# Performance work log

Measured on AMD Instinct MI355X. Metric: run time of the kernel, lower is better.

Reference implementation:

```python
import jax, jax.numpy as jnp
import numpy as np

N = 500_000      # total nodes in batched graph
B = 2_048        # number of graphs (segments)
D = 256          # input_dim == hidden_dim == output_dim


def setup_inputs() -> dict:
    key = jax.random.key(0)
    k = jax.random.split(key, 8)
    feat = jax.random.normal(k[0], (N, D), dtype=jnp.float32)
    cnt = jax.random.uniform(k[1], (N,), dtype=jnp.float32)
    segment_ids = jnp.sort(jax.random.randint(k[2], (N,), 0, B, dtype=jnp.int32))
    last_nodes = jax.random.randint(k[3], (B,), 0, N, dtype=jnp.int32)
    # learned parameters (torch nn.Linear: y = x @ W.T + b)
    s = 1.0 / np.sqrt(D)
    W_u = jax.random.uniform(k[4], (D, D), dtype=jnp.float32, minval=-s, maxval=s)
    W_v = jax.random.uniform(k[5], (D, D), dtype=jnp.float32, minval=-s, maxval=s)
    b_v = jax.random.uniform(k[6], (D,), dtype=jnp.float32, minval=-s, maxval=s)
    w_e = jax.random.uniform(k[7], (D,), dtype=jnp.float32, minval=-s, maxval=s)
    return {"feat": feat, "cnt": cnt, "segment_ids": segment_ids,
            "last_nodes": last_nodes, "W_u": W_u, "W_v": W_v,
            "b_v": b_v, "w_e": w_e}


def reference(feat, cnt, segment_ids, last_nodes, W_u, W_v, b_v, w_e):
    # fc_u: per-node projection  [N, D]
    feat_u = feat @ W_u.T
    # fc_v on last node of each graph, then broadcast back to nodes
    feat_v = feat[last_nodes] @ W_v.T + b_v          # [B, D]
    feat_vb = feat_v[segment_ids]                    # [N, D] broadcast_nodes
    # fc_e(sigmoid(u + v)) -> scalar gate per node
    e = jax.nn.sigmoid(feat_u + feat_vb) @ w_e       # [N]
    alpha = e * cnt                                  # [N]
    # segment-sum readout over graphs
    rst = jax.ops.segment_sum(feat * alpha[:, None], segment_ids,
                              num_segments=B)        # [B, D]
    return rst
```

## Files before the change

kernel.cpp:

```cpp
#include <hip/hip_runtime.h>
#include <hip/hip_bf16.h>

typedef __attribute__((ext_vector_type(8))) short short8;
typedef __attribute__((ext_vector_type(4))) float f32x4;

#define D 256
#define MT 64
#define NW 8
#define GRID_MAIN 512
#define G 16

__device__ __forceinline__ unsigned pack2(float a, float b) {
    __hip_bfloat162 h = __float22bfloat162_rn(make_float2(a, b));
    return *(unsigned*)&h;
}
__device__ __forceinline__ float fast_sigmoid(float x) {
    return __builtin_amdgcn_rcpf(1.f + __expf(-x));
}

__global__ __launch_bounds__(256) void k_prep(
    const float* __restrict__ W, unsigned short* __restrict__ Wb,
    float* __restrict__ rst, int nW, int nOut) {
    int b = blockIdx.x;
    if (b < 256) {
        int i = b * 256 + threadIdx.x;
        if (i < nW) Wb[i] = (unsigned short)(pack2(W[i], 0.f) & 0xffffu);
    } else {
        int i = (b - 256) * 256 + threadIdx.x;
        if (i < nOut) rst[i] = 0.f;
    }
}

__global__ __launch_bounds__(256) void k_featv(
    const float* __restrict__ feat, const int* __restrict__ last_nodes,
    const float* __restrict__ Wv, const float* __restrict__ bv,
    float* __restrict__ featv, int Bseg) {
    __shared__ float fln[G][D];
    const int t  = threadIdx.x;
    const int b0 = blockIdx.x * G;
    for (int g = 0; g < G; ++g) {
        int b = b0 + g;
        int ln = (b < Bseg) ? last_nodes[b] : 0;
        fln[g][t] = feat[(long)ln * D + t];
    }
    __syncthreads();
    float acc[G];
    float bvj = bv[t];
    #pragma unroll
    for (int g = 0; g < G; ++g) acc[g] = bvj;
    const float* wr = Wv + (long)t * D;
    for (int k = 0; k < D; k += 4) {
        float4 w4 = *(const float4*)(wr + k);
        #pragma unroll
        for (int g = 0; g < G; ++g) {
            acc[g] += w4.x * fln[g][k]     + w4.y * fln[g][k + 1]
                    + w4.z * fln[g][k + 2] + w4.w * fln[g][k + 3];
        }
    }
    for (int g = 0; g < G; ++g)
        if (b0 + g < Bseg) featv[(long)(b0 + g) * D + t] = acc[g];
}

__global__ __launch_bounds__(512, 2) void k_main(
    const float* __restrict__ feat, const float* __restrict__ cnt,
    const int* __restrict__ seg, const unsigned short* __restrict__ Wub,
    const float* __restrict__ featv, const float* __restrict__ we,
    float* __restrict__ rst, int N) {

    __shared__ unsigned short Abuf[2][MT][D];
    __shared__ float e_s[NW][MT];
    __shared__ int   seg_s[2][MT];
    __shared__ float cnt_s[2][MT];
    __shared__ float alpha_s[MT];

    const int t  = threadIdx.x;
    const int w  = t >> 6;
    const int l  = t & 63;
    const int rl = l & 15;
    const int h  = l >> 4;

    const int T   = (N + MT - 1) / MT;
    const int nb  = gridDim.x;
    const int per = T / nb, rem = T % nb;
    const int bid = blockIdx.x;
    const int c0  = bid * per + (bid < rem ? bid : rem);
    const int c1  = c0 + per + (bid < rem ? 1 : 0);
    if (c0 >= c1) return;

    short8 a_reg[2][8];
    {
        const unsigned short* ab = Wub + (long)(32 * w + rl) * D + h * 8;
        #pragma unroll
        for (int mt = 0; mt < 2; ++mt)
            #pragma unroll
            for (int s = 0; s < 8; ++s)
                a_reg[mt][s] = *(const short8*)(ab + (long)mt * 16 * D + s * 32);
    }
    f32x4 wev[2];
    wev[0] = *(const f32x4*)(we + 32 * w + h * 4);
    wev[1] = *(const f32x4*)(we + 32 * w + 16 + h * 4);

    {
        const long m0 = (long)c0 * MT;
        float4 sv[8];
        #pragma unroll
        for (int k = 0; k < 8; ++k) {
            long n = m0 + w * 8 + k; if (n > (long)N - 1) n = (long)N - 1;
            sv[k] = *(const float4*)(feat + n * D + 4 * l);
        }
        int sr = 0; float cr = 0.f;
        if (t < MT) {
            long n = m0 + t;
            if (n < N) { sr = seg[n]; cr = cnt[n]; }
            else       { sr = seg[N - 1]; cr = 0.f; }
        }
        #pragma unroll
        for (int k = 0; k < 8; ++k) {
            int R = w * 8 + k;
            uint2 v = make_uint2(pack2(sv[k].x, sv[k].y), pack2(sv[k].z, sv[k].w));
            *(uint2*)&Abuf[0][R][(((l >> 1) ^ k) << 3) + (l & 1) * 4] = v;
        }
        if (t < MT) { seg_s[0][t] = sr; cnt_s[0][t] = cr; }
        __syncthreads();
    }

    int cur = 0;
    for (int tt = c0; tt < c1; ++tt, cur ^= 1) {
        const int n0  = tt * MT;
        const int nv  = min(MT, N - n0);
        const bool more = (tt + 1 < c1);
        const int* seg_t = seg_s[cur];

        int sgv[4];
        #pragma unroll
        for (int nt = 0; nt < 4; ++nt) sgv[nt] = seg_t[nt * 16 + rl];

        f32x4 fvr[2][4];
        #pragma unroll
        for (int nt = 0; nt < 4; ++nt) {
            const float* fb = featv + (long)sgv[nt] * D + 32 * w + h * 4;
            fvr[0][nt] = *(const f32x4*)(fb);
            fvr[1][nt] = *(const f32x4*)(fb + 16);
        }
        asm volatile("" ::: "memory");

        float4 sv[8];
        int sr = 0; float cr = 0.f;
        if (more) {
            const long m1 = (long)(tt + 1) * MT;
            #pragma unroll
            for (int k = 0; k < 8; ++k) {
                long n = m1 + w * 8 + k; if (n > (long)N - 1) n = (long)N - 1;
                sv[k] = *(const float4*)(feat + n * D + 4 * l);
            }
            if (t < MT) {
                long n = m1 + t;
                if (n < N) { sr = seg[n]; cr = cnt[n]; }
                else       { sr = seg[N - 1]; cr = 0.f; }
            }
        }
        asm volatile("" ::: "memory");

        f32x4 acc[2][4];
        #pragma unroll
        for (int mt = 0; mt < 2; ++mt)
            #pragma unroll
            for (int nt = 0; nt < 4; ++nt) acc[mt][nt] = (f32x4)0.f;

        const unsigned short* Ab = &Abuf[cur][0][0];
        __builtin_amdgcn_s_setprio(1);
        #pragma unroll
        for (int s = 0; s < 8; ++s) {
            short8 bfr[4];
            #pragma unroll
            for (int nt = 0; nt < 4; ++nt) {
                int R = nt * 16 + rl;
                int gr = (s * 4 + h) ^ (rl & 7);
                bfr[nt] = *(const short8*)(Ab + R * D + gr * 8);
            }
            #pragma unroll
            for (int mt = 0; mt < 2; ++mt)
                #pragma unroll
                for (int nt = 0; nt < 4; ++nt)
                    acc[mt][nt] = __builtin_amdgcn_mfma_f32_16x16x32_bf16(a_reg[mt][s], bfr[nt], acc[mt][nt], 0, 0, 0);
        }
        __builtin_amdgcn_s_setprio(0);

        float ep[4] = {0.f, 0.f, 0.f, 0.f};
        #pragma unroll
        for (int mt = 0; mt < 2; ++mt)
            #pragma unroll
            for (int nt = 0; nt < 4; ++nt)
                #pragma unroll
                for (int r = 0; r < 4; ++r)
                    ep[nt] += wev[mt][r] * fast_sigmoid(acc[mt][nt][r] + fvr[mt][nt][r]);
        #pragma unroll
        for (int nt = 0; nt < 4; ++nt) {
            ep[nt] += __shfl_xor(ep[nt], 16);
            ep[nt] += __shfl_xor(ep[nt], 32);
        }
        if (h == 0) {
            #pragma unroll
            for (int nt = 0; nt < 4; ++nt) e_s[w][nt * 16 + rl] = ep[nt];
        }
        asm volatile("s_waitcnt lgkmcnt(0)\ns_barrier" ::: "memory");

        if (t < MT) {
            float e = 0.f;
            #pragma unroll
            for (int q = 0; q < NW; ++q) e += e_s[q][t];
            alpha_s[t] = e * cnt_s[cur][t];
        }
        asm volatile("s_waitcnt lgkmcnt(0)\ns_barrier" ::: "memory");

        if (more) {
            #pragma unroll
            for (int k = 0; k < 8; ++k) {
                int R = w * 8 + k;
                uint2 v = make_uint2(pack2(sv[k].x, sv[k].y), pack2(sv[k].z, sv[k].w));
                *(uint2*)&Abuf[cur ^ 1][R][(((l >> 1) ^ k) << 3) + (l & 1) * 4] = v;
            }
            if (t < MT) { seg_s[cur ^ 1][t] = sr; cnt_s[cur ^ 1][t] = cr; }
        }

        {
            const int p   = t & 127;
            const int gq  = t >> 7;
            const int i0  = gq * 16;
            const int i1v = min(i0 + 16, nv);
            const unsigned* Ab32 = (const unsigned*)Ab;
            if (i0 < i1v) {
                if ((i1v - i0) == 16 && seg_t[i0] == seg_t[i1v - 1]) {
                    float ca = 0.f, cb = 0.f, ca2 = 0.f, cb2 = 0.f;
                    #pragma unroll
                    for (int i2 = 0; i2 < 16; i2 += 2) {
                        int i = i0 + i2;
                        unsigned v0 = Ab32[(i + 0) * 128 + (((p >> 2) ^ ((i + 0) & 7)) << 2) + (p & 3)];
                        unsigned v1 = Ab32[(i + 1) * 128 + (((p >> 2) ^ ((i + 1) & 7)) << 2) + (p & 3)];
                        float a0 = alpha_s[i + 0], a1 = alpha_s[i + 1];
                        ca  += __uint_as_float(v0 << 16) * a0;
                        cb  += __uint_as_float(v0 & 0xffff0000u) * a0;
                        ca2 += __uint_as_float(v1 << 16) * a1;
                        cb2 += __uint_as_float(v1 & 0xffff0000u) * a1;
                    }
                    long rb = (long)seg_t[i0] * D + 2 * p;
                    atomicAdd(&rst[rb],     ca + ca2);
                    atomicAdd(&rst[rb + 1], cb + cb2);
                } else {
                    float ca = 0.f, cb = 0.f;
                    int curseg = seg_t[i0];
                    for (int i = i0; i < i1v; ++i) {
                        int sgi = seg_t[i];
                        if (sgi != curseg) {
                            long rb = (long)curseg * D + 2 * p;
                            atomicAdd(&rst[rb], ca); atomicAdd(&rst[rb + 1], cb);
                            ca = cb = 0.f; curseg = sgi;
                        }
                        unsigned v = Ab32[i * 128 + (((p >> 2) ^ (i & 7)) << 2) + (p & 3)];
                        float al = alpha_s[i];
                        ca += __uint_as_float(v << 16) * al;
                        cb += __uint_as_float(v & 0xffff0000u) * al;
                    }
                    long rb = (long)curseg * D + 2 * p;
                    atomicAdd(&rst[rb], ca); atomicAdd(&rst[rb + 1], cb);
                }
            }
        }
        asm volatile("s_waitcnt lgkmcnt(0)\ns_barrier" ::: "memory");
    }
}

extern "C" void kernel_launch(void* const* d_in, const int* in_sizes, int n_in,
                              void* d_out, int out_size, void* d_ws, size_t ws_size,
                              hipStream_t stream) {
    const float* feat = (const float*)d_in[0];
    const float* cnt  = (const float*)d_in[1];
    const int*   segp = (const int*)d_in[2];
    const int*   last = (const int*)d_in[3];
    const float* Wu   = (const float*)d_in[4];
    const float* Wv   = (const float*)d_in[5];
    const float* bv   = (const float*)d_in[6];
    const float* we   = (const float*)d_in[7];
    float* rst = (float*)d_out;

    const int N    = in_sizes[1];
    const int Bseg = in_sizes[3];

    unsigned short* Wub   = (unsigned short*)d_ws;
    float*          featv = (float*)((char*)d_ws + (size_t)D * D * sizeof(unsigned short));

    const int zero_blocks = (out_size + 255) / 256;
    k_prep<<<256 + zero_blocks, 256, 0, stream>>>(Wu, Wub, rst, D * D, out_size);
    k_featv<<<(Bseg + G - 1) / G, 256, 0, stream>>>(feat, last, Wv, bv, featv, Bseg);
    k_main<<<GRID_MAIN, 512, 0, stream>>>(feat, cnt, segp, Wub, featv, we, rst, N);
}
```

Baseline: 199.4 us.

## Stream feat tiles into LDS via async global_load_lds with two-deep prefetch

Replaces register-staged feat loads plus bf16 packing into LDS with direct global-to-LDS DMA of fp32 tiles into a ring buffer, prefetching two tiles ahead and converting to bf16 when reading MFMA operands. It also prefetches the next tile's featv rows, halves the main grid to 256 blocks, and merges the prep and featv kernels into one launch. The aim is to hide HBM latency and cut VGPR pressure and store instructions. In exchange LDS use doubles because tiles are held in fp32, conversion work moves into the inner loop, and correctness depends on hand-written vmcnt waits.

```diff
diff --git a/kernel.cpp b/kernel.cpp
--- a/kernel.cpp
+++ b/kernel.cpp
@@ -7,58 +7,67 @@
 #define D 256
 #define MT 64
 #define NW 8
-#define GRID_MAIN 512
-#define G 16
+#define GRID_MAIN 256
+#define GV 16
 
 __device__ __forceinline__ unsigned pack2(float a, float b) {
-    __hip_bfloat162 h = __float22bfloat162_rn(make_float2(a, b));
-    return *(unsigned*)&h;
+    __hip_bfloat162 hh = __float22bfloat162_rn(make_float2(a, b));
+    return *(unsigned*)&hh;
 }
 __device__ __forceinline__ float fast_sigmoid(float x) {
     return __builtin_amdgcn_rcpf(1.f + __expf(-x));
 }
+__device__ __forceinline__ void dma16(const void* g, void* lds) {
+    __builtin_amdgcn_global_load_lds((const __attribute__((address_space(1))) unsigned int*)g,
+                                     (__attribute__((address_space(3))) unsigned int*)lds, 16, 0, 0);
+}
+__device__ __forceinline__ void dma4(const void* g, void* lds) {
+    __builtin_amdgcn_global_load_lds((const __attribute__((address_space(1))) unsigned int*)g,
+                                     (__attribute__((address_space(3))) unsigned int*)lds, 4, 0, 0);
+}
 
 __global__ __launch_bounds__(256) void k_prep(
-    const float* __restrict__ W, unsigned short* __restrict__ Wb,
-    float* __restrict__ rst, int nW, int nOut) {
-    int b = blockIdx.x;
-    if (b < 256) {
-        int i = b * 256 + threadIdx.x;
-        if (i < nW) Wb[i] = (unsigned short)(pack2(W[i], 0.f) & 0xffffu);
-    } else {
-        int i = (b - 256) * 256 + threadIdx.x;
-        if (i < nOut) rst[i] = 0.f;
-    }
-}
-
-__global__ __launch_bounds__(256) void k_featv(
     const float* __restrict__ feat, const int* __restrict__ last_nodes,
     const float* __restrict__ Wv, const float* __restrict__ bv,
-    float* __restrict__ featv, int Bseg) {
-    __shared__ float fln[G][D];
-    const int t  = threadIdx.x;
-    const int b0 = blockIdx.x * G;
-    for (int g = 0; g < G; ++g) {
-        int b = b0 + g;
-        int ln = (b < Bseg) ? last_nodes[b] : 0;
-        fln[g][t] = feat[(long)ln * D + t];
-    }
-    __syncthreads();
-    float acc[G];
-    float bvj = bv[t];
-    #pragma unroll
-    for (int g = 0; g < G; ++g) acc[g] = bvj;
-    const float* wr = Wv + (long)t * D;
-    for (int k = 0; k < D; k += 4) {
-        float4 w4 = *(const float4*)(wr + k);
-        #pragma unroll
-        for (int g = 0; g < G; ++g) {
-            acc[g] += w4.x * fln[g][k]     + w4.y * fln[g][k + 1]
-                    + w4.z * fln[g][k + 2] + w4.w * fln[g][k + 3];
-        }
-    }
-    for (int g = 0; g < G; ++g)
-        if (b0 + g < Bseg) featv[(long)(b0 + g) * D + t] = acc[g];
+    const float* __restrict__ Wu, unsigned short* __restrict__ Wub,
+    float* __restrict__ featv, float* __restrict__ rst, int Bseg, int nOut) {
+    const int b = blockIdx.x;
+    const int t = threadIdx.x;
+    if (b < 128) {
+        __shared__ float fln[GV][D];
+        const int b0 = b * GV;
+        for (int g = 0; g < GV; ++g) {
+            int bb = b0 + g;
+            int ln = (bb < Bseg) ? last_nodes[bb] : 0;
+            fln[g][t] = feat[(long)ln * D + t];
+        }
+        __syncthreads();
+        float acc[GV];
+        float bvj = bv[t];
+        #pragma unroll
+        for (int g = 0; g < GV; ++g) acc[g] = bvj;
+        const float* wr = Wv + (long)t * D;
+        for (int k = 0; k < D; k += 4) {
+            float4 w4 = *(const float4*)(wr + k);
+            #pragma unroll
+            for (int g = 0; g < GV; ++g) {
+                acc[g] += w4.x * fln[g][k]     + w4.y * fln[g][k + 1]
+                        + w4.z * fln[g][k + 2] + w4.w * fln[g][k + 3];
+            }
+        }
+        for (int g = 0; g < GV; ++g)
+            if (b0 + g < Bseg) featv[(long)(b0 + g) * D + t] = acc[g];
+    } else if (b < 384) {
+        int i = (b - 128) * 256 + t;
+        if (i < D * D) Wub[i] = (unsigned short)(pack2(Wu[i], 0.f) & 0xffffu);
+    } else {
+        int base = (b - 384) * 1024 + t;
+        #pragma unroll
+        for (int it = 0; it < 4; ++it) {
+            int i = base + it * 256;
+            if (i < nOut) rst[i] = 0.f;
+        }
+    }
 }
 
 __global__ __launch_bounds__(512, 2) void k_main(
@@ -67,10 +76,10 @@
     const float* __restrict__ featv, const float* __restrict__ we,
     float* __restrict__ rst, int N) {
 
-    __shared__ unsigned short Abuf[2][MT][D];
-    __shared__ float e_s[NW][MT];
+    __shared__ float ring[4][MT * 128];
     __shared__ int   seg_s[2][MT];
     __shared__ float cnt_s[2][MT];
+    __shared__ float e_s[NW][MT];
     __shared__ float alpha_s[MT];
 
     const int t  = threadIdx.x;
@@ -87,6 +96,22 @@
     const int c1  = c0 + per + (bid < rem ? 1 : 0);
     if (c0 >= c1) return;
 
+#define STAGE_BATCH(sl, n0base)                                               \
+    {                                                                         \
+        long nsx = (n0base) + l; if (nsx > (long)N - 1) nsx = (long)N - 1;    \
+        dma4(seg + nsx, &seg_s[(sl)][0]);                                     \
+        dma4(cnt + nsx, &cnt_s[(sl)][0]);                                     \
+        _Pragma("unroll")                                                     \
+        for (int q = 0; q < 4; ++q) {                                         \
+            int ii = w + 8 * q;                                               \
+            int rr = 2 * ii + (l >> 5);                                       \
+            long nn = (n0base) + rr; if (nn > (long)N - 1) nn = (long)N - 1;  \
+            const float* srcp = feat + nn * D + 4 * ((l & 31) ^ (rr & 7));    \
+            dma16(srcp,       &ring[2 * (sl)][ii * 256]);                     \
+            dma16(srcp + 128, &ring[2 * (sl) + 1][ii * 256]);                 \
+        }                                                                     \
+    }
+
     short8 a_reg[2][8];
     {
         const unsigned short* ab = Wub + (long)(32 * w + rl) * D + h * 8;
@@ -100,66 +125,35 @@
     wev[0] = *(const f32x4*)(we + 32 * w + h * 4);
     wev[1] = *(const f32x4*)(we + 32 * w + 16 + h * 4);
 
+    f32x4 fvr[2][4];
+    STAGE_BATCH(0, (long)c0 * MT);
+    asm volatile("" ::: "memory");
+    asm volatile("s_waitcnt vmcnt(8)" ::: "memory");
     {
-        const long m0 = (long)c0 * MT;
-        float4 sv[8];
-        #pragma unroll
-        for (int k = 0; k < 8; ++k) {
-            long n = m0 + w * 8 + k; if (n > (long)N - 1) n = (long)N - 1;
-            sv[k] = *(const float4*)(feat + n * D + 4 * l);
-        }
-        int sr = 0; float cr = 0.f;
-        if (t < MT) {
-            long n = m0 + t;
-            if (n < N) { sr = seg[n]; cr = cnt[n]; }
-            else       { sr = seg[N - 1]; cr = 0.f; }
-        }
-        #pragma unroll
-        for (int k = 0; k < 8; ++k) {
-            int R = w * 8 + k;
-            uint2 v = make_uint2(pack2(sv[k].x, sv[k].y), pack2(sv[k].z, sv[k].w));
-            *(uint2*)&Abuf[0][R][(((l >> 1) ^ k) << 3) + (l & 1) * 4] = v;
-        }
-        if (t < MT) { seg_s[0][t] = sr; cnt_s[0][t] = cr; }
-        __syncthreads();
-    }
-
-    int cur = 0;
-    for (int tt = c0; tt < c1; ++tt, cur ^= 1) {
-        const int n0  = tt * MT;
-        const int nv  = min(MT, N - n0);
-        const bool more = (tt + 1 < c1);
-        const int* seg_t = seg_s[cur];
-
-        int sgv[4];
-        #pragma unroll
-        for (int nt = 0; nt < 4; ++nt) sgv[nt] = seg_t[nt * 16 + rl];
-
-        f32x4 fvr[2][4];
         #pragma unroll
         for (int nt = 0; nt < 4; ++nt) {
-            const float* fb = featv + (long)sgv[nt] * D + 32 * w + h * 4;
+            int sg = seg_s[0][nt * 16 + rl];
+            const float* fb = featv + (long)sg * D + 32 * w + h * 4;
             fvr[0][nt] = *(const f32x4*)(fb);
             fvr[1][nt] = *(const f32x4*)(fb + 16);
         }
-        asm volatile("" ::: "memory");
-
-        float4 sv[8];
-        int sr = 0; float cr = 0.f;
-        if (more) {
-            const long m1 = (long)(tt + 1) * MT;
-            #pragma unroll
-            for (int k = 0; k < 8; ++k) {
-                long n = m1 + w * 8 + k; if (n > (long)N - 1) n = (long)N - 1;
-                sv[k] = *(const float4*)(feat + n * D + 4 * l);
-            }
-            if (t < MT) {
-                long n = m1 + t;
-                if (n < N) { sr = seg[n]; cr = cnt[n]; }
-                else       { sr = seg[N - 1]; cr = 0.f; }
-            }
-        }
-        asm volatile("" ::: "memory");
+    }
+    asm volatile("" ::: "memory");
+    if (c0 + 1 < c1) STAGE_BATCH(1, (long)(c0 + 1) * MT);
+    asm volatile("" ::: "memory");
+
+    int slot = 0;
+    for (int tt = c0; tt < c1; ++tt, slot ^= 1) {
+        const long n0 = (long)tt * MT;
+        const bool more1 = (tt + 1 < c1);
+
+        if (more1) asm volatile("s_waitcnt vmcnt(8)" ::: "memory");
+        else       asm volatile("s_waitcnt vmcnt(0)" ::: "memory");
+        asm volatile("s_barrier" ::: "memory");
+
+        const float* bufL = &ring[2 * slot][0];
+        const float* bufH = &ring[2 * slot + 1][0];
+        const int* seg_t = seg_s[slot];
 
         f32x4 acc[2][4];
         #pragma unroll
@@ -167,16 +161,22 @@
             #pragma unroll
             for (int nt = 0; nt < 4; ++nt) acc[mt][nt] = (f32x4)0.f;
 
-        const unsigned short* Ab = &Abuf[cur][0][0];
         __builtin_amdgcn_s_setprio(1);
         #pragma unroll
         for (int s = 0; s < 8; ++s) {
+            const float* B = (s < 4) ? bufL : bufH;
+            const int s4 = s & 3;
             short8 bfr[4];
             #pragma unroll
             for (int nt = 0; nt < 4; ++nt) {
-                int R = nt * 16 + rl;
-                int gr = (s * 4 + h) ^ (rl & 7);
-                bfr[nt] = *(const short8*)(Ab + R * D + gr * 8);
+                int R  = nt * 16 + rl;
+                int g1 = 8 * s4 + 2 * h;
+                f32x4 lo = *(const f32x4*)(B + R * 128 + (((g1)     ^ (R & 7)) << 2));
+                f32x4 hi = *(const f32x4*)(B + R * 128 + (((g1 + 1) ^ (R & 7)) << 2));
+                union { unsigned u[4]; short8 s8; } cv;
+                cv.u[0] = pack2(lo[0], lo[1]); cv.u[1] = pack2(lo[2], lo[3]);
+                cv.u[2] = pack2(hi[0], hi[1]); cv.u[3] = pack2(hi[2], hi[3]);
+                bfr[nt] = cv.s8;
             }
             #pragma unroll
             for (int mt = 0; mt < 2; ++mt)
@@ -186,6 +186,19 @@
         }
         __builtin_amdgcn_s_setprio(0);
 
+        f32x4 fvn[2][4];
+        if (more1) {
+            const int* sn = seg_s[slot ^ 1];
+            #pragma unroll
+            for (int nt = 0; nt < 4; ++nt) {
+                int sg = sn[nt * 16 + rl];
+                const float* fb = featv + (long)sg * D + 32 * w + h * 4;
+                fvn[0][nt] = *(const f32x4*)(fb);
+                fvn[1][nt] = *(const f32x4*)(fb + 16);
+            }
+            asm volatile("" ::: "memory");
+        }
+
         float ep[4] = {0.f, 0.f, 0.f, 0.f};
         #pragma unroll
         for (int mt = 0; mt < 2; ++mt)
@@ -209,39 +222,29 @@
             float e = 0.f;
             #pragma unroll
             for (int q = 0; q < NW; ++q) e += e_s[q][t];
-            alpha_s[t] = e * cnt_s[cur][t];
+            alpha_s[t] = ((long)n0 + t < N) ? e * cnt_s[slot][t] : 0.f;
         }
         asm volatile("s_waitcnt lgkmcnt(0)\ns_barrier" ::: "memory");
-
-        if (more) {
-            #pragma unroll
-            for (int k = 0; k < 8; ++k) {
-                int R = w * 8 + k;
-                uint2 v = make_uint2(pack2(sv[k].x, sv[k].y), pack2(sv[k].z, sv[k].w));
-                *(uint2*)&Abuf[cur ^ 1][R][(((l >> 1) ^ k) << 3) + (l & 1) * 4] = v;
-            }
-            if (t < MT) { seg_s[cur ^ 1][t] = sr; cnt_s[cur ^ 1][t] = cr; }
-        }
 
         {
             const int p   = t & 127;
             const int gq  = t >> 7;
             const int i0  = gq * 16;
-            const int i1v = min(i0 + 16, nv);
-            const unsigned* Ab32 = (const unsigned*)Ab;
-            if (i0 < i1v) {
-                if ((i1v - i0) == 16 && seg_t[i0] == seg_t[i1v - 1]) {
+            const int nv  = (int)(((long)N - n0 < MT) ? ((long)N - n0) : MT);
+            const int i1  = (i0 + 16 < nv) ? i0 + 16 : nv;
+            const float* Bp = (p < 64) ? bufL : bufH;
+            const int p6 = p & 63;
+            if (i0 < i1) {
+                if ((i1 - i0) == 16 && seg_t[i0] == seg_t[i1 - 1]) {
                     float ca = 0.f, cb = 0.f, ca2 = 0.f, cb2 = 0.f;
                     #pragma unroll
                     for (int i2 = 0; i2 < 16; i2 += 2) {
                         int i = i0 + i2;
-                        unsigned v0 = Ab32[(i + 0) * 128 + (((p >> 2) ^ ((i + 0) & 7)) << 2) + (p & 3)];
-                        unsigned v1 = Ab32[(i + 1) * 128 + (((p >> 2) ^ ((i + 1) & 7)) << 2) + (p & 3)];
-                        float a0 = alpha_s[i + 0], a1 = alpha_s[i + 1];
-                        ca  += __uint_as_float(v0 << 16) * a0;
-                        cb  += __uint_as_float(v0 & 0xffff0000u) * a0;
-                        ca2 += __uint_as_float(v1 << 16) * a1;
-                        cb2 += __uint_as_float(v1 & 0xffff0000u) * a1;
+                        float2 v0 = *(const float2*)(Bp + (i)     * 128 + ((((p6 >> 1) ^ ((i)     & 7))) << 2) + (p & 1) * 2);
+                        float2 v1 = *(const float2*)(Bp + (i + 1) * 128 + ((((p6 >> 1) ^ ((i + 1) & 7))) << 2) + (p & 1) * 2);
+                        float a0 = alpha_s[i], a1 = alpha_s[i + 1];
+                        ca  += v0.x * a0; cb  += v0.y * a0;
+                        ca2 += v1.x * a1; cb2 += v1.y * a1;
                     }
                     long rb = (long)seg_t[i0] * D + 2 * p;
                     atomicAdd(&rst[rb],     ca + ca2);
@@ -249,17 +252,16 @@
                 } else {
                     float ca = 0.f, cb = 0.f;
                     int curseg = seg_t[i0];
-                    for (int i = i0; i < i1v; ++i) {
+                    for (int i = i0; i < i1; ++i) {
                         int sgi = seg_t[i];
                         if (sgi != curseg) {
                             long rb = (long)curseg * D + 2 * p;
                             atomicAdd(&rst[rb], ca); atomicAdd(&rst[rb + 1], cb);
                             ca = cb = 0.f; curseg = sgi;
                         }
-                        unsigned v = Ab32[i * 128 + (((p >> 2) ^ (i & 7)) << 2) + (p & 3)];
+                        float2 v = *(const float2*)(Bp + i * 128 + ((((p6 >> 1) ^ (i & 7))) << 2) + (p & 1) * 2);
                         float al = alpha_s[i];
-                        ca += __uint_as_float(v << 16) * al;
-                        cb += __uint_as_float(v & 0xffff0000u) * al;
+                        ca += v.x * al; cb += v.y * al;
                     }
                     long rb = (long)curseg * D + 2 * p;
                     atomicAdd(&rst[rb], ca); atomicAdd(&rst[rb + 1], cb);
@@ -267,7 +269,19 @@
             }
         }
         asm volatile("s_waitcnt lgkmcnt(0)\ns_barrier" ::: "memory");
-    }
+
+        if (tt + 2 < c1) {
+            STAGE_BATCH(slot, (long)(tt + 2) * MT);
+            asm volatile("" ::: "memory");
+        }
+        if (more1) {
+            #pragma unroll
+            for (int mt = 0; mt < 2; ++mt)
+                #pragma unroll
+                for (int nt = 0; nt < 4; ++nt) fvr[mt][nt] = fvn[mt][nt];
+        }
+    }
+#undef STAGE_BATCH
 }
 
 extern "C" void kernel_launch(void* const* d_in, const int* in_sizes, int n_in,
@@ -289,8 +303,6 @@
     unsigned short* Wub   = (unsigned short*)d_ws;
     float*          featv = (float*)((char*)d_ws + (size_t)D * D * sizeof(unsigned short));
 
-    const int zero_blocks = (out_size + 255) / 256;
-    k_prep<<<256 + zero_blocks, 256, 0, stream>>>(Wu, Wub, rst, D * D, out_size);
-    k_featv<<<(Bseg + G - 1) / G, 256, 0, stream>>>(feat, last, Wv, bv, featv, Bseg);
+    k_prep<<<896, 256, 0, stream>>>(feat, last, Wv, bv, Wu, Wub, featv, rst, Bseg, out_size);
     k_main<<<GRID_MAIN, 512, 0, stream>>>(feat, cnt, segp, Wub, featv, we, rst, N);
 }
```

New measurement: 252.3 us. 1.27x slower.
